# Kernel tuning notes

Measured on AMD Instinct MI355X. Metric: run time of the kernel, lower is better.

Reference implementation:

```python
import jax, jax.numpy as jnp
import numpy as np

N_NODES = 100000
N_EDGES = 1600000
F_IN = 64
HID = 64
N_CLASSES = 47


def lgconv(x, src, dst, n_nodes):
    # PyG LGConv: symmetric gcn_norm WITHOUT self-loops, sum aggregation.
    ones = jnp.ones(src.shape[0], dtype=x.dtype)
    deg = jax.ops.segment_sum(ones, dst, num_segments=n_nodes)  # in-degree at targets
    dinv = jnp.where(deg > 0, jax.lax.rsqrt(jnp.maximum(deg, 1.0)), 0.0)
    norm = dinv[src] * dinv[dst]  # [E]
    msg = x[src] * norm[:, None]  # [E, F] gathered messages
    return jax.ops.segment_sum(msg, dst, num_segments=n_nodes)  # [N, F]


def setup_inputs() -> dict:
    key = jax.random.key(0)
    k1, k2, k3, k4 = jax.random.split(key, 4)
    x = jax.random.normal(k1, (N_NODES, F_IN), dtype=jnp.float32)
    edge_index = jax.random.randint(k2, (2, N_EDGES), 0, N_NODES, dtype=jnp.int64)
    W1 = jax.random.normal(k3, (F_IN, HID), dtype=jnp.float32) * (1.0 / np.sqrt(F_IN))
    b1 = jnp.zeros((HID,), dtype=jnp.float32)
    W2 = jax.random.normal(k4, (HID, N_CLASSES), dtype=jnp.float32) * (1.0 / np.sqrt(HID))
    b2 = jnp.zeros((N_CLASSES,), dtype=jnp.float32)
    return {"x": x, "edge_index": edge_index, "W1": W1, "b1": b1, "W2": W2, "b2": b2}


def reference(x, edge_index, W1, b1, W2, b2):
    src, dst = edge_index[0], edge_index[1]
    h = jax.nn.relu(lgconv(x, src, dst, N_NODES))          # conv1 + relu (dropout = id in eval)
    h = jax.nn.relu(h @ W1 + b1)                           # lin1 + relu
    h = jax.nn.relu(lgconv(h, src, dst, N_NODES))          # conv2 + relu
    logits = h @ W2 + b2                                   # lin2
    return jax.nn.log_softmax(logits, axis=-1)
```

## Files before the change

kernel.cpp:

```cpp
#include <hip/hip_runtime.h>
#include <hip/hip_fp16.h>
#include <math.h>

#define NN 100000
#define F 64
#define NC 47
#define NSUP 98
#define SUPR 1024
#define ACHUNK 4096
#define PAD 24576

__global__ void detect_kernel(const void* __restrict__ ei, int* __restrict__ flag) {
    const int* e32 = (const int*)ei;
    int i = threadIdx.x;
    int v = e32[2 * i + 1];
    unsigned long long ball = __ballot(v == 0);
    if (i == 0) *flag = (ball == ~0ULL) ? 1 : 0;
}

__global__ __launch_bounds__(256) void binA_direct_kernel(const void* __restrict__ ei,
                                                          const int* __restrict__ flag,
                                                          int* __restrict__ superCnt,
                                                          unsigned* __restrict__ superArr,
                                                          int E) {
    __shared__ int2 ed[ACHUNK];
    __shared__ int h[128], gbase[128];
    int t = threadIdx.x;
    if (t < 128) h[t] = 0;
    __syncthreads();
    int cb = blockIdx.x * ACHUNK;
    int ce = min(cb + ACHUNK, E);
    bool is64 = (*flag != 0);
    for (int i = cb + t; i < ce; i += 256) {
        int s, d;
        if (is64) {
            s = (int)((const long long*)ei)[i];
            d = (int)((const long long*)ei)[(size_t)E + i];
        } else {
            s = ((const int*)ei)[i];
            d = ((const int*)ei)[(size_t)E + i];
        }
        ed[i - cb] = make_int2(s, d);
        atomicAdd(&h[d >> 10], 1);
    }
    __syncthreads();
    if (t < 128) {
        int c = h[t];
        gbase[t] = (t < NSUP && c > 0) ? atomicAdd(&superCnt[t], c) : 0;
        h[t] = 0;
    }
    __syncthreads();
    int nloc = ce - cb;
    for (int i = t; i < nloc; i += 256) {
        int2 e = ed[i];
        int sup = e.y >> 10;
        int pos = atomicAdd(&h[sup], 1);
        unsigned pk = (unsigned)e.x | ((unsigned)(e.y & (SUPR - 1)) << 17);
        superArr[(size_t)sup * PAD + gbase[sup] + pos] = pk;
    }
}

__global__ __launch_bounds__(128) void superscan_kernel(const int* __restrict__ superCnt,
                                                        int* __restrict__ superBase) {
    __shared__ int sc[128];
    int t = threadIdx.x;
    int v = (t < NSUP) ? superCnt[t] : 0;
    sc[t] = v;
    __syncthreads();
    for (int off = 1; off < 128; off <<= 1) {
        int a = (t >= off) ? sc[t - off] : 0;
        __syncthreads();
        sc[t] += a;
        __syncthreads();
    }
    if (t < NSUP) superBase[t] = sc[t] - v;
    if (t == NSUP - 1) superBase[NSUP] = sc[t];
}

__global__ __launch_bounds__(1024) void binB_fused_kernel(const unsigned* __restrict__ superArr,
                                                          const int* __restrict__ superCnt,
                                                          const int* __restrict__ superBase,
                                                          int* __restrict__ rowptr,
                                                          float* __restrict__ dinv,
                                                          unsigned* __restrict__ esrc, int E) {
    __shared__ int hist[SUPR];
    __shared__ int sc[SUPR];
    int s = blockIdx.x, t = threadIdx.x;
    int cnt = superCnt[s];
    int wb = superBase[s];
    const unsigned* arr = superArr + (size_t)s * PAD;
    int gr = s * SUPR + t;
    hist[t] = 0;
    __syncthreads();
    for (int i = t; i < cnt; i += 1024)
        atomicAdd(&hist[(arr[i] >> 17) & (SUPR - 1)], 1);
    __syncthreads();
    int myv = hist[t];
    sc[t] = myv;
    __syncthreads();
    for (int off = 1; off < 1024; off <<= 1) {
        int a = (t >= off) ? sc[t - off] : 0;
        __syncthreads();
        sc[t] += a;
        __syncthreads();
    }
    int excl = sc[t] - myv;
    if (gr < NN) {
        rowptr[gr] = wb + excl;
        dinv[gr] = (myv > 0) ? rsqrtf((float)myv) : 0.0f;
    }
    if (s == NSUP - 1 && t == 0) rowptr[NN] = E;
    __syncthreads();
    hist[t] = excl;
    __syncthreads();
    for (int i = t; i < cnt; i += 1024) {
        unsigned e = arr[i];
        int r = (e >> 17) & (SUPR - 1);
        int pos = atomicAdd(&hist[r], 1);
        esrc[wb + pos] = e & 0x1FFFFu;
    }
}

__global__ void f2h_scale_kernel(const float4* __restrict__ in4,
                                 const float* __restrict__ dinv,
                                 uint2* __restrict__ outh, int n4) {
    int i = blockIdx.x * blockDim.x + threadIdx.x;
    if (i >= n4) return;
    float dv = dinv[i >> 4];
    float4 v = in4[i];
    __half2 h01 = __floats2half2_rn(v.x * dv, v.y * dv);
    __half2 h23 = __floats2half2_rn(v.z * dv, v.w * dv);
    uint2 r;
    r.x = *(const unsigned*)&h01;
    r.y = *(const unsigned*)&h23;
    outh[i] = r;
}

__global__ __launch_bounds__(256) void conv_ps_kernel(const uint2* __restrict__ xh,
                                                      const int* __restrict__ rowptr,
                                                      const unsigned* __restrict__ esrc,
                                                      const float* __restrict__ dinv,
                                                      float4* __restrict__ out4, int n) {
    int row = blockIdx.x * 4 + (threadIdx.x >> 6);
    if (row >= n) return;
    int lane = threadIdx.x & 63;
    int es = lane >> 4, f4 = lane & 15;
    int beg = rowptr[row], end = rowptr[row + 1];
    float4 acc = make_float4(0.f, 0.f, 0.f, 0.f);
    for (int base = beg; base < end; base += 64) {
        int m = end - base;
        if (m > 64) m = 64;
        int pk = (lane < m) ? (int)esrc[base + lane] : 0;
        int iters = (m + 3) >> 2;
        int k = 0;
        for (; k + 2 <= iters; k += 2) {
            int i0 = 4 * k + es, i1 = i0 + 4;
            int s0 = __shfl(pk, i0, 64);
            int s1 = __shfl(pk, i1, 64);
            float w0 = (i0 < m) ? 1.0f : 0.0f;
            float w1 = (i1 < m) ? 1.0f : 0.0f;
            uint2 v0 = xh[(size_t)s0 * 16 + f4];
            uint2 v1 = xh[(size_t)s1 * 16 + f4];
            float2 a01 = __half22float2(*reinterpret_cast<const __half2*>(&v0.x));
            float2 a23 = __half22float2(*reinterpret_cast<const __half2*>(&v0.y));
            float2 b01 = __half22float2(*reinterpret_cast<const __half2*>(&v1.x));
            float2 b23 = __half22float2(*reinterpret_cast<const __half2*>(&v1.y));
            acc.x = fmaf(a01.x, w0, acc.x); acc.y = fmaf(a01.y, w0, acc.y);
            acc.z = fmaf(a23.x, w0, acc.z); acc.w = fmaf(a23.y, w0, acc.w);
            acc.x = fmaf(b01.x, w1, acc.x); acc.y = fmaf(b01.y, w1, acc.y);
            acc.z = fmaf(b23.x, w1, acc.z); acc.w = fmaf(b23.y, w1, acc.w);
        }
        if (k < iters) {
            int i0 = 4 * k + es;
            int s0 = __shfl(pk, i0, 64);
            float w0 = (i0 < m) ? 1.0f : 0.0f;
            uint2 v0 = xh[(size_t)s0 * 16 + f4];
            float2 a01 = __half22float2(*reinterpret_cast<const __half2*>(&v0.x));
            float2 a23 = __half22float2(*reinterpret_cast<const __half2*>(&v0.y));
            acc.x = fmaf(a01.x, w0, acc.x); acc.y = fmaf(a01.y, w0, acc.y);
            acc.z = fmaf(a23.x, w0, acc.z); acc.w = fmaf(a23.y, w0, acc.w);
        }
    }
#pragma unroll
    for (int off = 16; off <= 32; off <<= 1) {
        acc.x += __shfl_xor(acc.x, off, 64);
        acc.y += __shfl_xor(acc.y, off, 64);
        acc.z += __shfl_xor(acc.z, off, 64);
        acc.w += __shfl_xor(acc.w, off, 64);
    }
    if (es == 0) {
        float dv = dinv[row];
        acc.x *= dv; acc.y *= dv; acc.z *= dv; acc.w *= dv;
        out4[(size_t)row * 16 + f4] = acc;
    }
}

__device__ __forceinline__ float4 relu4(float4 v) {
    v.x = fmaxf(v.x, 0.0f); v.y = fmaxf(v.y, 0.0f);
    v.z = fmaxf(v.z, 0.0f); v.w = fmaxf(v.w, 0.0f);
    return v;
}

__global__ __launch_bounds__(256) void lin1_kernel(const float* __restrict__ h,
                                                   const float* __restrict__ W1,
                                                   const float* __restrict__ b1,
                                                   const float* __restrict__ dinv,
                                                   __half* __restrict__ outh, int n) {
    __shared__ float wt[64 * 64];
    __shared__ float ht[64 * 64];
    int t = threadIdx.x;
    for (int i = t; i < 64 * 64; i += 256) {
        int k = i >> 6, c = i & 63;
        int kq = k >> 2, slot = kq ^ (c & 7);
        wt[c * 64 + slot * 4 + (k & 3)] = W1[i];
    }
    int row0 = blockIdx.x * 64;
    const float4* h4 = (const float4*)h;
    float4* ht4 = (float4*)ht;
#pragma unroll
    for (int j = 0; j < 4; ++j) {
        int flat = t + 256 * j;
        int r = flat >> 4;
        int kq = flat & 15;
        int gr = row0 + r;
        float4 v = (gr < n) ? relu4(h4[(size_t)gr * 16 + kq])
                            : make_float4(0.f, 0.f, 0.f, 0.f);
        ht4[r * 16 + (kq ^ ((r >> 2) & 7))] = v;
    }
    __syncthreads();
    const float4* wt4 = (const float4*)wt;
    const float4* ht4c = (const float4*)ht;

    int tx = t & 15, ty = t >> 4;
    float acc[4][4] = {};
#pragma unroll 2
    for (int kq = 0; kq < 16; ++kq) {
        int wslot = kq ^ (tx & 7);
        float4 b0 = wt4[(tx +  0) * 16 + wslot];
        float4 b1v = wt4[(tx + 16) * 16 + wslot];
        float4 b2v = wt4[(tx + 32) * 16 + wslot];
        float4 b3v = wt4[(tx + 48) * 16 + wslot];
        int aslot = kq ^ (ty & 7);
#pragma unroll
        for (int i = 0; i < 4; ++i) {
            float4 a = ht4c[(4 * ty + i) * 16 + aslot];
            acc[i][0] = fmaf(a.x, b0.x,  fmaf(a.y, b0.y,  fmaf(a.z, b0.z,  fmaf(a.w, b0.w,  acc[i][0]))));
            acc[i][1] = fmaf(a.x, b1v.x, fmaf(a.y, b1v.y, fmaf(a.z, b1v.z, fmaf(a.w, b1v.w, acc[i][1]))));
            acc[i][2] = fmaf(a.x, b2v.x, fmaf(a.y, b2v.y, fmaf(a.z, b2v.z, fmaf(a.w, b2v.w, acc[i][2]))));
            acc[i][3] = fmaf(a.x, b3v.x, fmaf(a.y, b3v.y, fmaf(a.z, b3v.z, fmaf(a.w, b3v.w, acc[i][3]))));
        }
    }
    float bj[4];
#pragma unroll
    for (int g = 0; g < 4; ++g) bj[g] = b1[tx + 16 * g];
    int r0 = row0 + 4 * ty;
#pragma unroll
    for (int i = 0; i < 4; ++i) {
        int r = r0 + i;
        if (r >= n) break;
        float dv = dinv[r];
#pragma unroll
        for (int g = 0; g < 4; ++g)
            outh[(size_t)r * 64 + tx + 16 * g] =
                __float2half(fmaxf(acc[i][g] + bj[g], 0.0f) * dv);
    }
}

__global__ __launch_bounds__(256) void lin2_kernel(const float* __restrict__ h,
                                                   const float* __restrict__ W2,
                                                   const float* __restrict__ b2,
                                                   float* __restrict__ out, int n) {
    __shared__ float wt[64 * 64];
    __shared__ float ht[64 * 64];
    int t = threadIdx.x;
    for (int i = t; i < 64 * 64; i += 256) {
        int k = i >> 6, c = i & 63;
        int kq = k >> 2, slot = kq ^ (c & 7);
        wt[c * 64 + slot * 4 + (k & 3)] = (c < NC) ? W2[k * NC + c] : 0.0f;
    }
    int row0 = blockIdx.x * 64;
    const float4* h4 = (const float4*)h;
    float4* ht4 = (float4*)ht;
#pragma unroll
    for (int j = 0; j < 4; ++j) {
        int flat = t + 256 * j;
        int r = flat >> 4;
        int kq = flat & 15;
        int gr = row0 + r;
        float4 v = (gr < n) ? relu4(h4[(size_t)gr * 16 + kq])
                            : make_float4(0.f, 0.f, 0.f, 0.f);
        ht4[r * 16 + (kq ^ ((r >> 2) & 7))] = v;
    }
    __syncthreads();
    const float4* wt4 = (const float4*)wt;
    const float4* ht4c = (const float4*)ht;

    int tx = t & 15, ty = t >> 4;
    float acc[4][4] = {};
#pragma unroll 2
    for (int kq = 0; kq < 16; ++kq) {
        int wslot = kq ^ (tx & 7);
        float4 b0 = wt4[(tx +  0) * 16 + wslot];
        float4 b1v = wt4[(tx + 16) * 16 + wslot];
        float4 b2v = wt4[(tx + 32) * 16 + wslot];
        float4 b3v = wt4[(tx + 48) * 16 + wslot];
        int aslot = kq ^ (ty & 7);
#pragma unroll
        for (int i = 0; i < 4; ++i) {
            float4 a = ht4c[(4 * ty + i) * 16 + aslot];
            acc[i][0] = fmaf(a.x, b0.x,  fmaf(a.y, b0.y,  fmaf(a.z, b0.z,  fmaf(a.w, b0.w,  acc[i][0]))));
            acc[i][1] = fmaf(a.x, b1v.x, fmaf(a.y, b1v.y, fmaf(a.z, b1v.z, fmaf(a.w, b1v.w, acc[i][1]))));
            acc[i][2] = fmaf(a.x, b2v.x, fmaf(a.y, b2v.y, fmaf(a.z, b2v.z, fmaf(a.w, b2v.w, acc[i][2]))));
            acc[i][3] = fmaf(a.x, b3v.x, fmaf(a.y, b3v.y, fmaf(a.z, b3v.z, fmaf(a.w, b3v.w, acc[i][3]))));
        }
    }
    bool vm[4];
    float bj[4];
#pragma unroll
    for (int g = 0; g < 4; ++g) {
        int c = tx + 16 * g;
        vm[g] = (c < NC);
        bj[g] = vm[g] ? b2[c] : 0.0f;
    }
    int r0 = row0 + 4 * ty;
#pragma unroll
    for (int i = 0; i < 4; ++i) {
        int r = r0 + i;
        float v[4];
        float m = -INFINITY;
#pragma unroll
        for (int g = 0; g < 4; ++g) {
            v[g] = acc[i][g] + bj[g];
            if (vm[g]) m = fmaxf(m, v[g]);
        }
#pragma unroll
        for (int off = 8; off > 0; off >>= 1) m = fmaxf(m, __shfl_xor(m, off, 64));
        float s = 0.0f;
#pragma unroll
        for (int g = 0; g < 4; ++g)
            if (vm[g]) s += expf(v[g] - m);
#pragma unroll
        for (int off = 8; off > 0; off >>= 1) s += __shfl_xor(s, off, 64);
        float lse = m + logf(s);
        if (r < n) {
#pragma unroll
            for (int g = 0; g < 4; ++g)
                if (vm[g]) out[(size_t)r * NC + tx + 16 * g] = v[g] - lse;
        }
    }
}

extern "C" void kernel_launch(void* const* d_in, const int* in_sizes, int n_in,
                              void* d_out, int out_size, void* d_ws, size_t ws_size,
                              hipStream_t stream) {
    const float* x  = (const float*)d_in[0];
    const void*  ei = d_in[1];
    const float* W1 = (const float*)d_in[2];
    const float* b1 = (const float*)d_in[3];
    const float* W2 = (const float*)d_in[4];
    const float* b2 = (const float*)d_in[5];
    float* out = (float*)d_out;

    const int E = in_sizes[1] / 2;

    char* ws = (char*)d_ws;
    size_t off = 0;
    auto alloc = [&](size_t bytes) -> void* {
        void* p = ws + off;
        off = (off + bytes + 255) & ~(size_t)255;
        return p;
    };
    int*      flag      = (int*)     alloc(4);
    float*    dinv      = (float*)   alloc((size_t)NN * 4);
    int*      superCnt  = (int*)     alloc(128 * 4);
    int*      superBase = (int*)     alloc(132 * 4);
    unsigned* superArr  = (unsigned*)alloc((size_t)NSUP * PAD * 4);
    int*      rowptr    = (int*)     alloc((size_t)(NN + 1) * 4);
    unsigned* esrc      = (unsigned*)alloc((size_t)E * 4);
    uint2*    xh        = (uint2*)   alloc((size_t)NN * 16 * 8);
    __half*   bufBh     = (__half*)  alloc((size_t)NN * F * 2);
    float*    bufA      = (float*)   alloc((size_t)NN * F * 4);

    hipMemsetAsync(superCnt, 0, 128 * 4, stream);

    detect_kernel<<<1, 64, 0, stream>>>(ei, flag);

    binA_direct_kernel<<<(E + ACHUNK - 1) / ACHUNK, 256, 0, stream>>>(
        ei, flag, superCnt, superArr, E);
    superscan_kernel<<<1, 128, 0, stream>>>(superCnt, superBase);
    binB_fused_kernel<<<NSUP, 1024, 0, stream>>>(
        superArr, superCnt, superBase, rowptr, dinv, esrc, E);

    f2h_scale_kernel<<<(NN * 16 + 255) / 256, 256, 0, stream>>>(
        (const float4*)x, dinv, xh, NN * 16);

    const int conv_blocks = (NN + 3) / 4;
    const int lin_blocks = (NN + 63) / 64;

    conv_ps_kernel<<<conv_blocks, 256, 0, stream>>>(xh, rowptr, esrc, dinv,
                                                    (float4*)bufA, NN);

    lin1_kernel<<<lin_blocks, 256, 0, stream>>>(bufA, W1, b1, dinv, bufBh, NN);

    conv_ps_kernel<<<conv_blocks, 256, 0, stream>>>((const uint2*)bufBh, rowptr, esrc,
                                                    dinv, (float4*)bufA, NN);

    lin2_kernel<<<lin_blocks, 256, 0, stream>>>(bufA, W2, b2, out, NN);
}
```

Measured before the change: 188.6 us.

## Store conv outputs in fp16, fold tiny kernels, unroll gather by four

```diff
diff --git a/kernel.cpp b/kernel.cpp
--- a/kernel.cpp
+++ b/kernel.cpp
@@ -10,27 +10,24 @@
 #define ACHUNK 4096
 #define PAD 24576
 
-__global__ void detect_kernel(const void* __restrict__ ei, int* __restrict__ flag) {
-    const int* e32 = (const int*)ei;
-    int i = threadIdx.x;
-    int v = e32[2 * i + 1];
-    unsigned long long ball = __ballot(v == 0);
-    if (i == 0) *flag = (ball == ~0ULL) ? 1 : 0;
-}
-
 __global__ __launch_bounds__(256) void binA_direct_kernel(const void* __restrict__ ei,
-                                                          const int* __restrict__ flag,
                                                           int* __restrict__ superCnt,
                                                           unsigned* __restrict__ superArr,
                                                           int E) {
     __shared__ int2 ed[ACHUNK];
     __shared__ int h[128], gbase[128];
+    __shared__ int is64_s;
     int t = threadIdx.x;
+    if (t < 64) {
+        int v = ((const int*)ei)[2 * t + 1];
+        unsigned long long ball = __ballot(v == 0);
+        if (t == 0) is64_s = (ball == ~0ULL) ? 1 : 0;
+    }
     if (t < 128) h[t] = 0;
     __syncthreads();
+    bool is64 = (is64_s != 0);
     int cb = blockIdx.x * ACHUNK;
     int ce = min(cb + ACHUNK, E);
-    bool is64 = (*flag != 0);
     for (int i = cb + t; i < ce; i += 256) {
         int s, d;
         if (is64) {
@@ -60,38 +57,26 @@
     }
 }
 
-__global__ __launch_bounds__(128) void superscan_kernel(const int* __restrict__ superCnt,
-                                                        int* __restrict__ superBase) {
-    __shared__ int sc[128];
-    int t = threadIdx.x;
-    int v = (t < NSUP) ? superCnt[t] : 0;
-    sc[t] = v;
-    __syncthreads();
-    for (int off = 1; off < 128; off <<= 1) {
-        int a = (t >= off) ? sc[t - off] : 0;
-        __syncthreads();
-        sc[t] += a;
-        __syncthreads();
-    }
-    if (t < NSUP) superBase[t] = sc[t] - v;
-    if (t == NSUP - 1) superBase[NSUP] = sc[t];
-}
-
 __global__ __launch_bounds__(1024) void binB_fused_kernel(const unsigned* __restrict__ superArr,
                                                           const int* __restrict__ superCnt,
-                                                          const int* __restrict__ superBase,
                                                           int* __restrict__ rowptr,
                                                           float* __restrict__ dinv,
                                                           unsigned* __restrict__ esrc, int E) {
     __shared__ int hist[SUPR];
     __shared__ int sc[SUPR];
+    __shared__ int wb_s;
     int s = blockIdx.x, t = threadIdx.x;
+    if (t == 0) {
+        int r = 0;
+        for (int i = 0; i < s; ++i) r += superCnt[i];
+        wb_s = r;
+    }
+    hist[t] = 0;
+    __syncthreads();
+    int wb = wb_s;
     int cnt = superCnt[s];
-    int wb = superBase[s];
     const unsigned* arr = superArr + (size_t)s * PAD;
     int gr = s * SUPR + t;
-    hist[t] = 0;
-    __syncthreads();
     for (int i = t; i < cnt; i += 1024)
         atomicAdd(&hist[(arr[i] >> 17) & (SUPR - 1)], 1);
     __syncthreads();
@@ -140,7 +125,7 @@
                                                       const int* __restrict__ rowptr,
                                                       const unsigned* __restrict__ esrc,
                                                       const float* __restrict__ dinv,
-                                                      float4* __restrict__ out4, int n) {
+                                                      uint2* __restrict__ outh, int n) {
     int row = blockIdx.x * 4 + (threadIdx.x >> 6);
     if (row >= n) return;
     int lane = threadIdx.x & 63;
@@ -153,24 +138,38 @@
         int pk = (lane < m) ? (int)esrc[base + lane] : 0;
         int iters = (m + 3) >> 2;
         int k = 0;
-        for (; k + 2 <= iters; k += 2) {
-            int i0 = 4 * k + es, i1 = i0 + 4;
+        for (; k + 4 <= iters; k += 4) {
+            int i0 = 4 * k + es, i1 = i0 + 4, i2 = i0 + 8, i3 = i0 + 12;
             int s0 = __shfl(pk, i0, 64);
             int s1 = __shfl(pk, i1, 64);
+            int s2 = __shfl(pk, i2, 64);
+            int s3 = __shfl(pk, i3, 64);
             float w0 = (i0 < m) ? 1.0f : 0.0f;
             float w1 = (i1 < m) ? 1.0f : 0.0f;
+            float w2 = (i2 < m) ? 1.0f : 0.0f;
+            float w3 = (i3 < m) ? 1.0f : 0.0f;
             uint2 v0 = xh[(size_t)s0 * 16 + f4];
             uint2 v1 = xh[(size_t)s1 * 16 + f4];
+            uint2 v2 = xh[(size_t)s2 * 16 + f4];
+            uint2 v3 = xh[(size_t)s3 * 16 + f4];
             float2 a01 = __half22float2(*reinterpret_cast<const __half2*>(&v0.x));
             float2 a23 = __half22float2(*reinterpret_cast<const __half2*>(&v0.y));
+            acc.x = fmaf(a01.x, w0, acc.x); acc.y = fmaf(a01.y, w0, acc.y);
+            acc.z = fmaf(a23.x, w0, acc.z); acc.w = fmaf(a23.y, w0, acc.w);
             float2 b01 = __half22float2(*reinterpret_cast<const __half2*>(&v1.x));
             float2 b23 = __half22float2(*reinterpret_cast<const __half2*>(&v1.y));
-            acc.x = fmaf(a01.x, w0, acc.x); acc.y = fmaf(a01.y, w0, acc.y);
-            acc.z = fmaf(a23.x, w0, acc.z); acc.w = fmaf(a23.y, w0, acc.w);
             acc.x = fmaf(b01.x, w1, acc.x); acc.y = fmaf(b01.y, w1, acc.y);
             acc.z = fmaf(b23.x, w1, acc.z); acc.w = fmaf(b23.y, w1, acc.w);
-        }
-        if (k < iters) {
+            float2 c01 = __half22float2(*reinterpret_cast<const __half2*>(&v2.x));
+            float2 c23 = __half22float2(*reinterpret_cast<const __half2*>(&v2.y));
+            acc.x = fmaf(c01.x, w2, acc.x); acc.y = fmaf(c01.y, w2, acc.y);
+            acc.z = fmaf(c23.x, w2, acc.z); acc.w = fmaf(c23.y, w2, acc.w);
+            float2 d01 = __half22float2(*reinterpret_cast<const __half2*>(&v3.x));
+            float2 d23 = __half22float2(*reinterpret_cast<const __half2*>(&v3.y));
+            acc.x = fmaf(d01.x, w3, acc.x); acc.y = fmaf(d01.y, w3, acc.y);
+            acc.z = fmaf(d23.x, w3, acc.z); acc.w = fmaf(d23.y, w3, acc.w);
+        }
+        for (; k < iters; ++k) {
             int i0 = 4 * k + es;
             int s0 = __shfl(pk, i0, 64);
             float w0 = (i0 < m) ? 1.0f : 0.0f;
@@ -190,18 +189,23 @@
     }
     if (es == 0) {
         float dv = dinv[row];
-        acc.x *= dv; acc.y *= dv; acc.z *= dv; acc.w *= dv;
-        out4[(size_t)row * 16 + f4] = acc;
-    }
-}
-
-__device__ __forceinline__ float4 relu4(float4 v) {
-    v.x = fmaxf(v.x, 0.0f); v.y = fmaxf(v.y, 0.0f);
-    v.z = fmaxf(v.z, 0.0f); v.w = fmaxf(v.w, 0.0f);
-    return v;
-}
-
-__global__ __launch_bounds__(256) void lin1_kernel(const float* __restrict__ h,
+        __half2 h01 = __floats2half2_rn(acc.x * dv, acc.y * dv);
+        __half2 h23 = __floats2half2_rn(acc.z * dv, acc.w * dv);
+        uint2 r;
+        r.x = *(const unsigned*)&h01;
+        r.y = *(const unsigned*)&h23;
+        outh[(size_t)row * 16 + f4] = r;
+    }
+}
+
+__device__ __forceinline__ float4 h4_to_f4_relu(uint2 hv) {
+    float2 a01 = __half22float2(*reinterpret_cast<const __half2*>(&hv.x));
+    float2 a23 = __half22float2(*reinterpret_cast<const __half2*>(&hv.y));
+    return make_float4(fmaxf(a01.x, 0.f), fmaxf(a01.y, 0.f),
+                       fmaxf(a23.x, 0.f), fmaxf(a23.y, 0.f));
+}
+
+__global__ __launch_bounds__(256) void lin1_kernel(const uint2* __restrict__ h2,
                                                    const float* __restrict__ W1,
                                                    const float* __restrict__ b1,
                                                    const float* __restrict__ dinv,
@@ -215,7 +219,6 @@
         wt[c * 64 + slot * 4 + (k & 3)] = W1[i];
     }
     int row0 = blockIdx.x * 64;
-    const float4* h4 = (const float4*)h;
     float4* ht4 = (float4*)ht;
 #pragma unroll
     for (int j = 0; j < 4; ++j) {
@@ -223,7 +226,7 @@
         int r = flat >> 4;
         int kq = flat & 15;
         int gr = row0 + r;
-        float4 v = (gr < n) ? relu4(h4[(size_t)gr * 16 + kq])
+        float4 v = (gr < n) ? h4_to_f4_relu(h2[(size_t)gr * 16 + kq])
                             : make_float4(0.f, 0.f, 0.f, 0.f);
         ht4[r * 16 + (kq ^ ((r >> 2) & 7))] = v;
     }
@@ -266,7 +269,7 @@
     }
 }
 
-__global__ __launch_bounds__(256) void lin2_kernel(const float* __restrict__ h,
+__global__ __launch_bounds__(256) void lin2_kernel(const uint2* __restrict__ h2,
                                                    const float* __restrict__ W2,
                                                    const float* __restrict__ b2,
                                                    float* __restrict__ out, int n) {
@@ -279,7 +282,6 @@
         wt[c * 64 + slot * 4 + (k & 3)] = (c < NC) ? W2[k * NC + c] : 0.0f;
     }
     int row0 = blockIdx.x * 64;
-    const float4* h4 = (const float4*)h;
     float4* ht4 = (float4*)ht;
 #pragma unroll
     for (int j = 0; j < 4; ++j) {
@@ -287,7 +289,7 @@
         int r = flat >> 4;
         int kq = flat & 15;
         int gr = row0 + r;
-        float4 v = (gr < n) ? relu4(h4[(size_t)gr * 16 + kq])
+        float4 v = (gr < n) ? h4_to_f4_relu(h2[(size_t)gr * 16 + kq])
                             : make_float4(0.f, 0.f, 0.f, 0.f);
         ht4[r * 16 + (kq ^ ((r >> 2) & 7))] = v;
     }
@@ -370,26 +372,21 @@
         off = (off + bytes + 255) & ~(size_t)255;
         return p;
     };
-    int*      flag      = (int*)     alloc(4);
     float*    dinv      = (float*)   alloc((size_t)NN * 4);
     int*      superCnt  = (int*)     alloc(128 * 4);
-    int*      superBase = (int*)     alloc(132 * 4);
     unsigned* superArr  = (unsigned*)alloc((size_t)NSUP * PAD * 4);
     int*      rowptr    = (int*)     alloc((size_t)(NN + 1) * 4);
     unsigned* esrc      = (unsigned*)alloc((size_t)E * 4);
     uint2*    xh        = (uint2*)   alloc((size_t)NN * 16 * 8);
+    __half*   bufAh     = (__half*)  alloc((size_t)NN * F * 2);
     __half*   bufBh     = (__half*)  alloc((size_t)NN * F * 2);
-    float*    bufA      = (float*)   alloc((size_t)NN * F * 4);
 
     hipMemsetAsync(superCnt, 0, 128 * 4, stream);
 
-    detect_kernel<<<1, 64, 0, stream>>>(ei, flag);
-
     binA_direct_kernel<<<(E + ACHUNK - 1) / ACHUNK, 256, 0, stream>>>(
-        ei, flag, superCnt, superArr, E);
-    superscan_kernel<<<1, 128, 0, stream>>>(superCnt, superBase);
+        ei, superCnt, superArr, E);
     binB_fused_kernel<<<NSUP, 1024, 0, stream>>>(
-        superArr, superCnt, superBase, rowptr, dinv, esrc, E);
+        superArr, superCnt, rowptr, dinv, esrc, E);
 
     f2h_scale_kernel<<<(NN * 16 + 255) / 256, 256, 0, stream>>>(
         (const float4*)x, dinv, xh, NN * 16);
@@ -398,12 +395,13 @@
     const int lin_blocks = (NN + 63) / 64;
 
     conv_ps_kernel<<<conv_blocks, 256, 0, stream>>>(xh, rowptr, esrc, dinv,
-                                                    (float4*)bufA, NN);
-
-    lin1_kernel<<<lin_blocks, 256, 0, stream>>>(bufA, W1, b1, dinv, bufBh, NN);
+                                                    (uint2*)bufAh, NN);
+
+    lin1_kernel<<<lin_blocks, 256, 0, stream>>>((const uint2*)bufAh, W1, b1, dinv,
+                                                bufBh, NN);
 
     conv_ps_kernel<<<conv_blocks, 256, 0, stream>>>((const uint2*)bufBh, rowptr, esrc,
-                                                    dinv, (float4*)bufA, NN);
-
-    lin2_kernel<<<lin_blocks, 256, 0, stream>>>(bufA, W2, b2, out, NN);
-}
+                                                    dinv, (uint2*)bufAh, NN);
+
+    lin2_kernel<<<lin_blocks, 256, 0, stream>>>((const uint2*)bufAh, W2, b2, out, NN);
+}
```

Result: faster. 181.1 us (-4.0%).
